# Performance work log

Hardware: AMD Instinct MI355X
Metric: run time of the kernel (lower is better)

## Reference

```python
import jax, jax.numpy as jnp
import numpy as np

N_NODES = 50000
N_EDGES = 800000
IN_DIM, HIDDEN, OUT_DIM, HEADS = 64, 32, 32, 4
NEG_SLOPE = 0.2  # PyG GATConv default negative_slope


def _glorot(key, shape):
    fan = shape[0] + shape[-1]
    lim = jnp.sqrt(6.0 / fan)
    return jax.random.uniform(key, shape, jnp.float32, -lim, lim)


def setup_inputs() -> dict:
    key = jax.random.key(0)
    ks = jax.random.split(key, 8)
    x = jax.random.normal(ks[0], (N_NODES, IN_DIM), jnp.float32)
    edge_index = jax.random.randint(ks[1], (2, N_EDGES), 0, N_NODES, jnp.int64)
    return {
        "x": x,
        "edge_index": edge_index,
        "W1": _glorot(ks[2], (IN_DIM, HEADS * HIDDEN)),
        "att_src1": _glorot(ks[3], (HEADS, HIDDEN)),
        "att_dst1": _glorot(ks[4], (HEADS, HIDDEN)),
        "b1": jnp.zeros((HEADS * HIDDEN,), jnp.float32),
        "W2": _glorot(ks[5], (HEADS * HIDDEN, OUT_DIM)),
        "att_src2": _glorot(ks[6], (1, OUT_DIM)),
        "att_dst2": _glorot(ks[7], (1, OUT_DIM)),
        "b2": jnp.zeros((OUT_DIM,), jnp.float32),
    }


def gat_conv(x, src, dst, W, att_src, att_dst, bias, concat):
    # PyG GATConv: linear per head, edge attention, segment softmax over dst, scatter-add.
    N = x.shape[0]
    heads, out = att_src.shape
    h = (x @ W).reshape(N, heads, out)                       # (N, H, O)
    a_s = jnp.einsum('nho,ho->nh', h, att_src)               # (N, H)
    a_d = jnp.einsum('nho,ho->nh', h, att_dst)
    e = jax.nn.leaky_relu(a_s[src] + a_d[dst], NEG_SLOPE)    # (E, H)
    # numerically-stable segment softmax over incoming edges of each dst node
    emax = jax.ops.segment_max(e, dst, num_segments=N)       # (N, H)
    ex = jnp.exp(e - emax[dst])
    denom = jax.ops.segment_sum(ex, dst, num_segments=N)
    alpha = ex / denom[dst]                                  # (E, H)
    msg = h[src] * alpha[:, :, None]                         # (E, H, O) gather + weight
    agg = jax.ops.segment_sum(msg, dst, num_segments=N)      # (N, H, O) scatter-add
    outp = agg.reshape(N, heads * out) if concat else agg.mean(axis=1)
    return outp + bias


def reference(x, edge_index, W1, att_src1, att_dst1, b1, W2, att_src2, att_dst2, b2):
    N = x.shape[0]
    # PyG GATConv adds self-loops by default
    loops = jnp.arange(N, dtype=edge_index.dtype)
    src = jnp.concatenate([edge_index[0], loops])
    dst = jnp.concatenate([edge_index[1], loops])
    h = gat_conv(x, src, dst, W1, att_src1, att_dst1, b1, concat=True)
    h = jax.nn.elu(h)
    return gat_conv(h, src, dst, W2, att_src2, att_dst2, b2, concat=False)
```

## Files before the change

kernel.cpp:

```cpp
#include <hip/hip_runtime.h>
#include <hip/hip_bf16.h>
#include <math.h>

#define N_NODES 50000
#define N_EDGES 800000
#define E_TOT   (N_EDGES + N_NODES)
#define NEG_SLOPE 0.2f
#define SLOT_CAP 64

__device__ __forceinline__ float lrelu(float x) { return x >= 0.f ? x : NEG_SLOPE * x; }
__device__ __forceinline__ float frcp(float x) { return __builtin_amdgcn_rcpf(x); }

__device__ __forceinline__ unsigned bf16r(float x) {
    unsigned u = __float_as_uint(x);
    return (u + 0x7fffu + ((u >> 16) & 1u)) >> 16;
}
__device__ __forceinline__ unsigned pack2(float lo, float hi) {
    return bf16r(lo) | (bf16r(hi) << 16);
}
__device__ __forceinline__ float bflo(unsigned u) { return __uint_as_float(u << 16); }
__device__ __forceinline__ float bfhi(unsigned u) { return __uint_as_float(u & 0xffff0000u); }

__global__ void bucket_edges(const int* __restrict__ ei, int* __restrict__ cnt,
                             int* __restrict__ slot) {
    int e = blockIdx.x * blockDim.x + threadIdx.x;
    if (e >= E_TOT) return;
    int s, d;
    if (e < N_EDGES) { s = ei[e]; d = ei[N_EDGES + e]; }
    else             { s = d = e - N_EDGES; }
    int pos = atomicAdd(&cnt[d], 1);
    if (pos < SLOT_CAP) slot[(size_t)pos * N_NODES + d] = s;
}

__global__ __launch_bounds__(256) void
gemm1(const float* __restrict__ x, const float* __restrict__ W1,
      const float* __restrict__ att_s, const float* __restrict__ att_d,
      unsigned* __restrict__ h1u, float* __restrict__ as1, float* __restrict__ ad1) {
    int t = threadIdx.x;
    int w = t >> 6, l = t & 63;
    int nbase = blockIdx.x * 64;

    __shared__ float W1s[64 * 128];
    __shared__ float xs[64][65];

    float4* W1sv = (float4*)W1s;
    const float4* W1v = (const float4*)W1;
    for (int i = t; i < 2048; i += 256) W1sv[i] = W1v[i];

    const float4* xv = (const float4*)(x + (size_t)nbase * 64);
    int nvalid = min(64, N_NODES - nbase);
    for (int i = t; i < nvalid * 16; i += 256) {
        float4 v = xv[i];
        int n = i >> 4, k4 = (i & 15) * 4;
        xs[n][k4] = v.x; xs[n][k4 + 1] = v.y; xs[n][k4 + 2] = v.z; xs[n][k4 + 3] = v.w;
    }
    __syncthreads();

    float acc[32];
#pragma unroll
    for (int e = 0; e < 32; ++e) acc[e] = 0.f;

#pragma unroll 8
    for (int k = 0; k < 64; ++k) {
        float xk = xs[l][k];
        const float4* wr = (const float4*)(W1s + k * 128 + w * 32);
#pragma unroll
        for (int e4 = 0; e4 < 8; ++e4) {
            float4 wv = wr[e4];
            acc[e4 * 4 + 0] += xk * wv.x;
            acc[e4 * 4 + 1] += xk * wv.y;
            acc[e4 * 4 + 2] += xk * wv.z;
            acc[e4 * 4 + 3] += xk * wv.w;
        }
    }

    int n = nbase + l;
    if (n < N_NODES) {
        uint4* hv = (uint4*)(h1u + (size_t)n * 64 + w * 16);
#pragma unroll
        for (int e4 = 0; e4 < 4; ++e4) {
            uint4 pk;
            pk.x = pack2(acc[e4 * 8 + 0], acc[e4 * 8 + 1]);
            pk.y = pack2(acc[e4 * 8 + 2], acc[e4 * 8 + 3]);
            pk.z = pack2(acc[e4 * 8 + 4], acc[e4 * 8 + 5]);
            pk.w = pack2(acc[e4 * 8 + 6], acc[e4 * 8 + 7]);
            hv[e4] = pk;
        }
        float ps = 0.f, pd = 0.f;
#pragma unroll
        for (int e = 0; e < 32; ++e) {
            ps += acc[e] * att_s[w * 32 + e];
            pd += acc[e] * att_d[w * 32 + e];
        }
        as1[n * 4 + w] = ps;
        ad1[n * 4 + w] = pd;
    }
}

__global__ void node_agg1(const int* __restrict__ cnt, const int* __restrict__ slot,
                          const float* __restrict__ as1, const float* __restrict__ ad1,
                          const uint4* __restrict__ h1q, const float* __restrict__ b1,
                          const float* __restrict__ W2, const float* __restrict__ att_s2,
                          const float* __restrict__ att_d2,
                          unsigned* __restrict__ h2u, float* __restrict__ as2,
                          float* __restrict__ ad2) {
    int tb = threadIdx.x;
    int wv = tb >> 6, t = tb & 63;
    int n = blockIdx.x * 2 + wv;
    int deg = min(cnt[n], SLOT_CAP);
    float4 ad = *(const float4*)(ad1 + n * 4);

    __shared__ float els[2][SLOT_CAP * 4];
    __shared__ int  slds[2][SLOT_CAP];
    __shared__ float hrow[2][128];

    {
        int ah = t & 3;
        float adh = (ah == 0) ? ad.x : (ah == 1) ? ad.y : (ah == 2) ? ad.z : ad.w;
        for (int p = (t >> 2); p < deg; p += 16) {
            int s = slot[(size_t)p * N_NODES + n];
            els[wv][p * 4 + ah] = __expf(lrelu(as1[s * 4 + ah] + adh));
            if (ah == 0) slds[wv][p] = s;
        }
    }
    __syncthreads();

    int oct = t & 15, g = t >> 4, hq = oct >> 2;
    float a0 = 0.f, a1 = 0.f, a2 = 0.f, a3 = 0.f;
    float a4 = 0.f, a5 = 0.f, a6 = 0.f, a7 = 0.f;
    float accE = 0.f;
    for (int p = g; p < deg; p += 4) {
        float ex = els[wv][p * 4 + hq];
        accE += ex;
        uint4 hv = h1q[(size_t)slds[wv][p] * 16 + oct];
        a0 += ex * bflo(hv.x); a1 += ex * bfhi(hv.x);
        a2 += ex * bflo(hv.y); a3 += ex * bfhi(hv.y);
        a4 += ex * bflo(hv.z); a5 += ex * bfhi(hv.z);
        a6 += ex * bflo(hv.w); a7 += ex * bfhi(hv.w);
    }
    for (int m = 16; m <= 32; m <<= 1) {
        a0 += __shfl_xor(a0, m, 64); a1 += __shfl_xor(a1, m, 64);
        a2 += __shfl_xor(a2, m, 64); a3 += __shfl_xor(a3, m, 64);
        a4 += __shfl_xor(a4, m, 64); a5 += __shfl_xor(a5, m, 64);
        a6 += __shfl_xor(a6, m, 64); a7 += __shfl_xor(a7, m, 64);
        accE += __shfl_xor(accE, m, 64);
    }
    {
        float rE = frcp(accE);
        const float4* b1v = (const float4*)b1;
        float4 bA = b1v[oct * 2], bB = b1v[oct * 2 + 1];
        float v0 = a0 * rE + bA.x, v1 = a1 * rE + bA.y;
        float v2 = a2 * rE + bA.z, v3 = a3 * rE + bA.w;
        float v4 = a4 * rE + bB.x, v5 = a5 * rE + bB.y;
        float v6 = a6 * rE + bB.z, v7 = a7 * rE + bB.w;
        v0 = v0 > 0.f ? v0 : __expf(v0) - 1.f;
        v1 = v1 > 0.f ? v1 : __expf(v1) - 1.f;
        v2 = v2 > 0.f ? v2 : __expf(v2) - 1.f;
        v3 = v3 > 0.f ? v3 : __expf(v3) - 1.f;
        v4 = v4 > 0.f ? v4 : __expf(v4) - 1.f;
        v5 = v5 > 0.f ? v5 : __expf(v5) - 1.f;
        v6 = v6 > 0.f ? v6 : __expf(v6) - 1.f;
        v7 = v7 > 0.f ? v7 : __expf(v7) - 1.f;
        if (g == 0) {
            float4* hw = (float4*)&hrow[wv][oct * 8];
            hw[0] = make_float4(v0, v1, v2, v3);
            hw[1] = make_float4(v4, v5, v6, v7);
        }
    }
    __syncthreads();

    {
        int l = t & 31, half = t >> 5;
        const float* hr = hrow[wv];
        int k0 = half * 64;
        float pacc = 0.f;
#pragma unroll 16
        for (int k = 0; k < 64; ++k)
            pacc += hr[k0 + k] * W2[(k0 + k) * 32 + l];
        pacc += __shfl_xor(pacc, 32, 64);
        float hv2 = pacc;
        float ps = hv2 * att_s2[l];
        float pd = hv2 * att_d2[l];
        for (int m = 16; m >= 1; m >>= 1) {
            ps += __shfl_xor(ps, m, 64);
            pd += __shfl_xor(pd, m, 64);
        }
        if (t == 0) { as2[n] = ps; ad2[n] = pd; }
        float hvn = __shfl_down(hv2, 1, 64);
        if (t < 32 && (t & 1) == 0)
            h2u[n * 16 + (t >> 1)] = pack2(hv2, hvn);
    }
}

__global__ void node_agg2(const int* __restrict__ cnt, const int* __restrict__ slot,
                          const float* __restrict__ as2, const float* __restrict__ ad2,
                          const uint2* __restrict__ h2d, const float* __restrict__ b2,
                          float* __restrict__ out) {
    int n = blockIdx.x;
    int t = threadIdx.x;
    int c = t & 7, g = t >> 3;
    int deg = min(cnt[n], SLOT_CAP);
    float ad = ad2[n];

    __shared__ float els[SLOT_CAP];
    __shared__ int  slds[SLOT_CAP];

    if (t < deg) {
        int s = slot[(size_t)t * N_NODES + n];
        els[t] = __expf(lrelu(as2[s] + ad));
        slds[t] = s;
    }
    __syncthreads();

    float a0 = 0.f, a1 = 0.f, a2 = 0.f, a3 = 0.f;
    float accE = 0.f;
#pragma unroll 2
    for (int p = g; p < deg; p += 8) {
        float ex = els[p];
        accE += ex;
        uint2 hv = h2d[(size_t)slds[p] * 8 + c];
        a0 += ex * bflo(hv.x); a1 += ex * bfhi(hv.x);
        a2 += ex * bflo(hv.y); a3 += ex * bfhi(hv.y);
    }
    for (int m = 8; m <= 32; m <<= 1) {
        a0 += __shfl_xor(a0, m, 64); a1 += __shfl_xor(a1, m, 64);
        a2 += __shfl_xor(a2, m, 64); a3 += __shfl_xor(a3, m, 64);
        accE += __shfl_xor(accE, m, 64);
    }
    if (t < 8) {
        float rE = frcp(accE);
        const float4* bb = (const float4*)(b2 + t * 4);
        float4 r = make_float4(a0 * rE + bb->x, a1 * rE + bb->y,
                               a2 * rE + bb->z, a3 * rE + bb->w);
        *(float4*)(out + n * 32 + t * 4) = r;
    }
}

extern "C" void kernel_launch(void* const* d_in, const int* in_sizes, int n_in,
                              void* d_out, int out_size, void* d_ws, size_t ws_size,
                              hipStream_t stream) {
    const float* x        = (const float*)d_in[0];
    const int*   ei       = (const int*)d_in[1];
    const float* W1       = (const float*)d_in[2];
    const float* att_src1 = (const float*)d_in[3];
    const float* att_dst1 = (const float*)d_in[4];
    const float* b1       = (const float*)d_in[5];
    const float* W2       = (const float*)d_in[6];
    const float* att_src2 = (const float*)d_in[7];
    const float* att_dst2 = (const float*)d_in[8];
    const float* b2       = (const float*)d_in[9];
    float* out = (float*)d_out;

    float* p = (float*)d_ws;
    unsigned* h1u = (unsigned*)p; p += N_NODES * 64;
    unsigned* h2u = (unsigned*)p; p += N_NODES * 16;
    float* as1   = p; p += N_NODES * 4;
    float* ad1   = p; p += N_NODES * 4;
    float* as2   = p; p += N_NODES;
    float* ad2   = p; p += N_NODES;
    int* ip = (int*)p;
    int* cnt   = ip; ip += N_NODES;
    int* slot  = ip; ip += N_NODES * SLOT_CAP;

    hipMemsetAsync(cnt, 0, N_NODES * sizeof(int), stream);

    bucket_edges<<<(E_TOT + 255) / 256, 256, 0, stream>>>(ei, cnt, slot);

    gemm1<<<(N_NODES + 63) / 64, 256, 0, stream>>>(x, W1, att_src1, att_dst1,
                                                   h1u, as1, ad1);

    node_agg1<<<N_NODES / 2, 128, 0, stream>>>(cnt, slot, as1, ad1,
                                               (const uint4*)h1u, b1,
                                               W2, att_src2, att_dst2, h2u, as2, ad2);

    node_agg2<<<N_NODES, 64, 0, stream>>>(cnt, slot, as2, ad2,
                                          (const uint2*)h2u, b2, out);
}
```

Measured before the change: 169.9 us.

## Fuse edge bucketing into GEMM launch and unroll gather loops by two

Merges the edge-bucketing kernel into the first GEMM kernel as extra blocks of one launch, removing one kernel launch and letting the two independent jobs run on the GPU at the same time. The GEMM now reads W1 straight from global memory, using a wave-uniform index, instead of staging it in shared memory, which cuts LDS use and the preload. Both aggregation loops now process two neighbors per iteration so more independent loads are in flight. Risks: W1 reads from global or L1 may be slower than LDS, and the predicated second load adds branches.

```diff
diff --git a/kernel.cpp b/kernel.cpp
--- a/kernel.cpp
+++ b/kernel.cpp
@@ -7,6 +7,8 @@
 #define E_TOT   (N_EDGES + N_NODES)
 #define NEG_SLOPE 0.2f
 #define SLOT_CAP 64
+#define GEMM_BLOCKS ((N_NODES + 63) / 64)
+#define BUCKET_BLOCKS ((E_TOT + 255) / 256)
 
 __device__ __forceinline__ float lrelu(float x) { return x >= 0.f ? x : NEG_SLOPE * x; }
 __device__ __forceinline__ float frcp(float x) { return __builtin_amdgcn_rcpf(x); }
@@ -21,31 +23,31 @@
 __device__ __forceinline__ float bflo(unsigned u) { return __uint_as_float(u << 16); }
 __device__ __forceinline__ float bfhi(unsigned u) { return __uint_as_float(u & 0xffff0000u); }
 
-__global__ void bucket_edges(const int* __restrict__ ei, int* __restrict__ cnt,
-                             int* __restrict__ slot) {
-    int e = blockIdx.x * blockDim.x + threadIdx.x;
-    if (e >= E_TOT) return;
-    int s, d;
-    if (e < N_EDGES) { s = ei[e]; d = ei[N_EDGES + e]; }
-    else             { s = d = e - N_EDGES; }
-    int pos = atomicAdd(&cnt[d], 1);
-    if (pos < SLOT_CAP) slot[(size_t)pos * N_NODES + d] = s;
-}
-
 __global__ __launch_bounds__(256) void
-gemm1(const float* __restrict__ x, const float* __restrict__ W1,
-      const float* __restrict__ att_s, const float* __restrict__ att_d,
-      unsigned* __restrict__ h1u, float* __restrict__ as1, float* __restrict__ ad1) {
+gemm1_bucket(const float* __restrict__ x, const float* __restrict__ W1,
+             const float* __restrict__ att_s, const float* __restrict__ att_d,
+             unsigned* __restrict__ h1u, float* __restrict__ as1,
+             float* __restrict__ ad1,
+             const int* __restrict__ ei, int* __restrict__ cnt,
+             int* __restrict__ slot) {
+    int b = blockIdx.x;
+    if (b >= GEMM_BLOCKS) {
+        int e = (b - GEMM_BLOCKS) * 256 + threadIdx.x;
+        if (e < E_TOT) {
+            int s, d;
+            if (e < N_EDGES) { s = ei[e]; d = ei[N_EDGES + e]; }
+            else             { s = d = e - N_EDGES; }
+            int pos = atomicAdd(&cnt[d], 1);
+            if (pos < SLOT_CAP) slot[(size_t)pos * N_NODES + d] = s;
+        }
+        return;
+    }
     int t = threadIdx.x;
-    int w = t >> 6, l = t & 63;
-    int nbase = blockIdx.x * 64;
-
-    __shared__ float W1s[64 * 128];
+    int w = __builtin_amdgcn_readfirstlane(t >> 6);
+    int l = t & 63;
+    int nbase = b * 64;
+
     __shared__ float xs[64][65];
-
-    float4* W1sv = (float4*)W1s;
-    const float4* W1v = (const float4*)W1;
-    for (int i = t; i < 2048; i += 256) W1sv[i] = W1v[i];
 
     const float4* xv = (const float4*)(x + (size_t)nbase * 64);
     int nvalid = min(64, N_NODES - nbase);
@@ -60,10 +62,10 @@
 #pragma unroll
     for (int e = 0; e < 32; ++e) acc[e] = 0.f;
 
-#pragma unroll 8
+#pragma unroll 4
     for (int k = 0; k < 64; ++k) {
         float xk = xs[l][k];
-        const float4* wr = (const float4*)(W1s + k * 128 + w * 32);
+        const float4* wr = (const float4*)(W1 + k * 128 + w * 32);
 #pragma unroll
         for (int e4 = 0; e4 < 8; ++e4) {
             float4 wv = wr[e4];
@@ -129,14 +131,26 @@
     float a0 = 0.f, a1 = 0.f, a2 = 0.f, a3 = 0.f;
     float a4 = 0.f, a5 = 0.f, a6 = 0.f, a7 = 0.f;
     float accE = 0.f;
-    for (int p = g; p < deg; p += 4) {
-        float ex = els[wv][p * 4 + hq];
-        accE += ex;
-        uint4 hv = h1q[(size_t)slds[wv][p] * 16 + oct];
-        a0 += ex * bflo(hv.x); a1 += ex * bfhi(hv.x);
-        a2 += ex * bflo(hv.y); a3 += ex * bfhi(hv.y);
-        a4 += ex * bflo(hv.z); a5 += ex * bfhi(hv.z);
-        a6 += ex * bflo(hv.w); a7 += ex * bfhi(hv.w);
+#pragma unroll 2
+    for (int p = g; p < deg; p += 8) {
+        float exA = els[wv][p * 4 + hq];
+        uint4 hvA = h1q[(size_t)slds[wv][p] * 16 + oct];
+        int pB = p + 4;
+        float exB = 0.f;
+        uint4 hvB = make_uint4(0u, 0u, 0u, 0u);
+        if (pB < deg) {
+            exB = els[wv][pB * 4 + hq];
+            hvB = h1q[(size_t)slds[wv][pB] * 16 + oct];
+        }
+        accE += exA + exB;
+        a0 += exA * bflo(hvA.x) + exB * bflo(hvB.x);
+        a1 += exA * bfhi(hvA.x) + exB * bfhi(hvB.x);
+        a2 += exA * bflo(hvA.y) + exB * bflo(hvB.y);
+        a3 += exA * bfhi(hvA.y) + exB * bfhi(hvB.y);
+        a4 += exA * bflo(hvA.z) + exB * bflo(hvB.z);
+        a5 += exA * bfhi(hvA.z) + exB * bfhi(hvB.z);
+        a6 += exA * bflo(hvA.w) + exB * bflo(hvB.w);
+        a7 += exA * bfhi(hvA.w) + exB * bfhi(hvB.w);
     }
     for (int m = 16; m <= 32; m <<= 1) {
         a0 += __shfl_xor(a0, m, 64); a1 += __shfl_xor(a1, m, 64);
@@ -214,13 +228,21 @@
 
     float a0 = 0.f, a1 = 0.f, a2 = 0.f, a3 = 0.f;
     float accE = 0.f;
-#pragma unroll 2
-    for (int p = g; p < deg; p += 8) {
-        float ex = els[p];
-        accE += ex;
-        uint2 hv = h2d[(size_t)slds[p] * 8 + c];
-        a0 += ex * bflo(hv.x); a1 += ex * bfhi(hv.x);
-        a2 += ex * bflo(hv.y); a3 += ex * bfhi(hv.y);
+    for (int p = g; p < deg; p += 16) {
+        float exA = els[p];
+        uint2 hvA = h2d[(size_t)slds[p] * 8 + c];
+        int pB = p + 8;
+        float exB = 0.f;
+        uint2 hvB = make_uint2(0u, 0u);
+        if (pB < deg) {
+            exB = els[pB];
+            hvB = h2d[(size_t)slds[pB] * 8 + c];
+        }
+        accE += exA + exB;
+        a0 += exA * bflo(hvA.x) + exB * bflo(hvB.x);
+        a1 += exA * bfhi(hvA.x) + exB * bfhi(hvB.x);
+        a2 += exA * bflo(hvA.y) + exB * bflo(hvB.y);
+        a3 += exA * bfhi(hvA.y) + exB * bfhi(hvB.y);
     }
     for (int m = 8; m <= 32; m <<= 1) {
         a0 += __shfl_xor(a0, m, 64); a1 += __shfl_xor(a1, m, 64);
@@ -264,10 +286,8 @@
 
     hipMemsetAsync(cnt, 0, N_NODES * sizeof(int), stream);
 
-    bucket_edges<<<(E_TOT + 255) / 256, 256, 0, stream>>>(ei, cnt, slot);
-
-    gemm1<<<(N_NODES + 63) / 64, 256, 0, stream>>>(x, W1, att_src1, att_dst1,
-                                                   h1u, as1, ad1);
+    gemm1_bucket<<<GEMM_BLOCKS + BUCKET_BLOCKS, 256, 0, stream>>>(
+        x, W1, att_src1, att_dst1, h1u, as1, ad1, ei, cnt, slot);
 
     node_agg1<<<N_NODES / 2, 128, 0, stream>>>(cnt, slot, as1, ad1,
                                                (const uint4*)h1u, b1,
```

New measurement: 137.4 us (median of 2 runs). -19.1%, faster.
